# Kernel optimization log

Measured on AMD Instinct MI355X. Metric: run time of the kernel, lower is better.

Reference implementation:

```python
import jax, jax.numpy as jnp
import numpy as np

B, C, OC, H, W = 2, 64, 128, 96, 96
HD, DI, N, R, K = C // 2, C, 16, 2, 4  # VSSBlock: hidden=C/2, d_inner=2*hidden=C, d_state, dt_rank, 4 scan dirs
EPS = 1e-5


def _conv(x, w, b, pad, groups=1):
    y = jax.lax.conv_general_dilated(x, w, (1, 1), pad, feature_group_count=groups,
                                     dimension_numbers=('NCHW', 'OIHW', 'NCHW'))
    return y + b[None, :, None, None]


def _ln(x, w, b):
    m = x.mean(-1, keepdims=True)
    v = x.var(-1, keepdims=True)
    return (x - m) * jax.lax.rsqrt(v + EPS) * w + b


def _selective_scan(xs, dts, Bs, Cs, A, D):
    # xs, dts: (B,K,DI,L); Bs, Cs: (B,K,N,L); A: (K,DI,N); D: (K,DI)
    dts = jax.nn.softplus(dts)

    def step(h, inp):
        u_t, dt_t, B_t, C_t = inp
        dA = jnp.exp(dt_t[..., None] * A)                         # (B,K,DI,N)
        h = dA * h + (dt_t * u_t)[..., None] * B_t[:, :, None, :]
        return h, jnp.einsum('bkdn,bkn->bkd', h, C_t)

    seq = (jnp.moveaxis(xs, -1, 0), jnp.moveaxis(dts, -1, 0),
           jnp.moveaxis(Bs, -1, 0), jnp.moveaxis(Cs, -1, 0))
    h0 = jnp.zeros(xs.shape[:3] + (A.shape[-1],), xs.dtype)
    _, ys = jax.lax.scan(step, h0, seq)
    return jnp.moveaxis(ys, 0, -1) + D[None, :, :, None] * xs


def _vss_block(x, ln_w, ln_b, in_w, conv_w, conv_b, xproj_w, dtproj_w, dtproj_b,
               A_logs, Ds, on_w, on_b, out_w):
    # x: (B,H,W,HD); VMamba SS2D with 4-direction cross-scan + residual
    b, hh, ww, _ = x.shape
    L = hh * ww
    h = _ln(x, ln_w, ln_b)
    xz = h @ in_w                                   # (B,H,W,2*DI)
    xp, z = jnp.split(xz, 2, axis=-1)
    xc = jnp.transpose(xp, (0, 3, 1, 2))            # (B,DI,H,W)
    xc = jax.nn.silu(_conv(xc, conv_w, conv_b, ((1, 1), (1, 1)), groups=DI))
    x_flat = xc.reshape(b, DI, L)
    x_wh = jnp.transpose(xc, (0, 1, 3, 2)).reshape(b, DI, L)
    x2 = jnp.stack([x_flat, x_wh], axis=1)
    xs = jnp.concatenate([x2, jnp.flip(x2, -1)], axis=1)      # (B,4,DI,L)
    x_dbl = jnp.einsum('bkdl,kcd->bkcl', xs, xproj_w)
    dts, Bs, Cs = jnp.split(x_dbl, [R, R + N], axis=2)
    dts = jnp.einsum('bkrl,kdr->bkdl', dts, dtproj_w) + dtproj_b[None, :, :, None]
    A = -jnp.exp(A_logs)
    ys = _selective_scan(xs, dts, Bs, Cs, A, Ds)              # (B,4,DI,L)
    inv = jnp.flip(ys[:, 2:4], -1)
    unwh = lambda t: jnp.transpose(t.reshape(b, DI, ww, hh), (0, 1, 3, 2)).reshape(b, DI, L)
    y = ys[:, 0] + inv[:, 0] + unwh(ys[:, 1]) + unwh(inv[:, 1])
    y = jnp.transpose(y.reshape(b, DI, hh, ww), (0, 2, 3, 1))
    y = _ln(y, on_w, on_b) * jax.nn.silu(z)
    return x + y @ out_w


def _forward(x, ms_dw33_w, ms_dw33_b, ms_in_w, ms_in_b, ms_scale,
             vss_ln_w, vss_ln_b, vss_in_w, vss_conv_w, vss_conv_b, vss_xproj_w,
             vss_dtproj_w, vss_dtproj_b, vss_A_logs, vss_Ds, vss_on_w, vss_on_b, vss_out_w,
             ma_conv_w, ma_conv_b, adw_h_w, adw_h_b, adw_w_w, adw_w_b,
             pw_w, pw_b, bn_w, bn_b, bn_mean, bn_var):
    vss = (vss_ln_w, vss_ln_b, vss_in_w, vss_conv_w, vss_conv_b, vss_xproj_w,
           vss_dtproj_w, vss_dtproj_b, vss_A_logs, vss_Ds, vss_on_w, vss_on_b, vss_out_w)
    # --- MambaSplit (shared VSSBlock applied to both channel halves) ---
    xd = _conv(x, ms_dw33_w, ms_dw33_b, ((1, 1), (1, 1)), groups=C)
    x1, x2 = jnp.split(xd, 2, axis=1)

    def branch(xp):
        y = _vss_block(jnp.transpose(xp, (0, 2, 3, 1)), *vss)
        return ms_scale * xp + jnp.transpose(y, (0, 3, 1, 2))

    xm = jnp.concatenate([branch(x1), branch(x2)], axis=1)
    m = xm.mean((2, 3), keepdims=True)
    v = xm.var((2, 3), keepdims=True)
    xm = (xm - m) * jax.lax.rsqrt(v + EPS) * ms_in_w[None, :, None, None] + ms_in_b[None, :, None, None]
    xm = jax.nn.leaky_relu(xm, 0.01)
    # --- MaxAvg (global avg+max pool -> 3x3 conv on 1x1 map -> sigmoid gate) ---
    pooled = jnp.concatenate([x.mean((2, 3), keepdims=True), x.max((2, 3), keepdims=True)], axis=1)
    gate = jax.nn.sigmoid(_conv(pooled, ma_conv_w, ma_conv_b, ((1, 1), (1, 1))))
    xs_ = xm + gate * x
    # --- AxialDW ---
    xs_ = xs_ + _conv(xs_, adw_h_w, adw_h_b, ((1, 1), (0, 0)), groups=C) \
              + _conv(xs_, adw_w_w, adw_w_b, ((0, 0), (1, 1)), groups=C)
    # --- BN (eval) + ReLU, 1x1 conv, 2x2 maxpool ---
    skip = jax.nn.relu((xs_ - bn_mean[None, :, None, None]) * jax.lax.rsqrt(bn_var[None, :, None, None] + EPS)
                       * bn_w[None, :, None, None] + bn_b[None, :, None, None])
    out = _conv(skip, pw_w, pw_b, ((0, 0), (0, 0)))
    down = jax.lax.reduce_window(out, -jnp.inf, jax.lax.max, (1, 1, 2, 2), (1, 1, 2, 2), 'VALID')
    return down, skip


def setup_inputs() -> dict:
    key = jax.random.key(0)
    ks = jax.random.split(key, 16)
    r = lambda i, shape, s=0.02: jax.random.normal(ks[i], shape, jnp.float32) * s
    return {
        'x': jax.random.normal(ks[0], (B, C, H, W), jnp.float32),
        'ms_dw33_w': r(1, (C, 1, 3, 3), 0.1), 'ms_dw33_b': jnp.zeros(C),
        'ms_in_w': jnp.ones(C), 'ms_in_b': jnp.zeros(C),
        'ms_scale': jnp.ones((1,)),
        'vss_ln_w': jnp.ones(HD), 'vss_ln_b': jnp.zeros(HD),
        'vss_in_w': r(2, (HD, 2 * DI)),
        'vss_conv_w': r(3, (DI, 1, 3, 3), 0.1), 'vss_conv_b': jnp.zeros(DI),
        'vss_xproj_w': r(4, (K, R + 2 * N, DI)),
        'vss_dtproj_w': r(5, (K, DI, R), 0.1), 'vss_dtproj_b': r(6, (K, DI), 0.1),
        'vss_A_logs': jnp.tile(jnp.log(jnp.arange(1, N + 1, dtype=jnp.float32)), (K, DI, 1)),
        'vss_Ds': jnp.ones((K, DI)),
        'vss_on_w': jnp.ones(DI), 'vss_on_b': jnp.zeros(DI),
        'vss_out_w': r(7, (DI, HD)),
        'ma_conv_w': r(8, (C, 2 * C, 3, 3), 0.05), 'ma_conv_b': jnp.zeros(C),
        'adw_h_w': r(9, (C, 1, 3, 1), 0.1), 'adw_h_b': jnp.zeros(C),
        'adw_w_w': r(10, (C, 1, 1, 3), 0.1), 'adw_w_b': jnp.zeros(C),
        'pw_w': r(11, (OC, C, 1, 1)), 'pw_b': jnp.zeros(OC),
        'bn_w': jnp.ones(C), 'bn_b': jnp.zeros(C),
        'bn_mean': jnp.zeros(C), 'bn_var': jnp.ones(C),
    }


def reference(x, ms_dw33_w, ms_dw33_b, ms_in_w, ms_in_b, ms_scale,
              vss_ln_w, vss_ln_b, vss_in_w, vss_conv_w, vss_conv_b, vss_xproj_w,
              vss_dtproj_w, vss_dtproj_b, vss_A_logs, vss_Ds, vss_on_w, vss_on_b, vss_out_w,
              ma_conv_w, ma_conv_b, adw_h_w, adw_h_b, adw_w_w, adw_w_b,
              pw_w, pw_b, bn_w, bn_b, bn_mean, bn_var):
    return _forward(x, ms_dw33_w, ms_dw33_b, ms_in_w, ms_in_b, ms_scale,
                    vss_ln_w, vss_ln_b, vss_in_w, vss_conv_w, vss_conv_b, vss_xproj_w,
                    vss_dtproj_w, vss_dtproj_b, vss_A_logs, vss_Ds, vss_on_w, vss_on_b, vss_out_w,
                    ma_conv_w, ma_conv_b, adw_h_w, adw_h_b, adw_w_w, adw_w_b,
                    pw_w, pw_b, bn_w, bn_b, bn_mean, bn_var)
```

## Files before the change

kernel.cpp:

```cpp
#include <hip/hip_runtime.h>
#include <hip/hip_bf16.h>

typedef __hip_bfloat16 bf16;
#define DEV __device__ __forceinline__

constexpr int B_ = 2, C_ = 64, H_ = 96, W_ = 96, L_ = 9216;
constexpr int HD_ = 32, DI_ = 64, N_ = 16, K_ = 4, BB_ = 4;
constexpr int OC_ = 128;
constexpr int CH_ = 384, CL_ = 24;
constexpr int XST = 36;
constexpr float EPSF = 1e-5f;
constexpr int DOWN_SZ = B_ * OC_ * 48 * 48;

typedef __attribute__((ext_vector_type(8))) short short8;
typedef __attribute__((ext_vector_type(4))) float f32x4;

DEV float softplusf(float x) { return x > 15.f ? x : __logf(1.f + __expf(x)); }
DEV float b2f(bf16 v) { return __bfloat162float(v); }

__constant__ float kLogN[16] = {
  0.0f, 0.69314718f, 1.09861229f, 1.38629436f, 1.60943791f, 1.79175947f,
  1.94591015f, 2.07944154f, 2.19722458f, 2.30258509f, 2.39789527f,
  2.48490665f, 2.56494936f, 2.63905733f, 2.70805020f, 2.77258872f};

DEV void chunk_addr(int k, int chunk, int& idx0, int& stride) {
  int r4 = chunk & 3, q = chunk >> 2;
  if (k == 0)      { idx0 = chunk * CL_;                        stride = 1;   }
  else if (k == 1) { idx0 = (24 * r4) * 96 + q;                 stride = 96;  }
  else if (k == 2) { idx0 = L_ - 1 - chunk * CL_;               stride = -1;  }
  else             { idx0 = (95 - 24 * r4) * 96 + (95 - q);     stride = -96; }
}

DEV void pow_tree(float e1, float* ep) {
  float e2 = e1 * e1, e4 = e2 * e2, e8 = e4 * e4;
  float e3 = e2 * e1, e5 = e4 * e1, e6 = e4 * e2, e7 = e4 * e3;
  ep[0] = e1;  ep[1] = e2;  ep[2] = e3;  ep[3] = e4;
  ep[4] = e5;  ep[5] = e6;  ep[6] = e7;  ep[7] = e8;
  ep[8] = e8 * e1;  ep[9] = e8 * e2;  ep[10] = e8 * e3;  ep[11] = e8 * e4;
  ep[12] = e8 * e5; ep[13] = e8 * e6; ep[14] = e8 * e7;  ep[15] = e8 * e8;
}

DEV void ld_b(const float* __restrict__ xdb, const bf16* __restrict__ xcb, int d, int idx,
              float& t0, float& t1, float& u, float* Bv) {
  int uidx = __builtin_amdgcn_readfirstlane(idx);
  const float* p = xdb + (size_t)uidx * XST;
  t0 = p[0]; t1 = p[1];
  u = b2f(xcb[(size_t)idx * DI_ + d]);
  *(float4*)&Bv[0]  = *(const float4*)(p + 4);
  *(float4*)&Bv[4]  = *(const float4*)(p + 8);
  *(float4*)&Bv[8]  = *(const float4*)(p + 12);
  *(float4*)&Bv[12] = *(const float4*)(p + 16);
}
DEV void ld_bc(const float* __restrict__ xdb, const bf16* __restrict__ xcb, int d, int idx,
               float& t0, float& t1, float& u, float* Bv, float* Cv) {
  int uidx = __builtin_amdgcn_readfirstlane(idx);
  const float* p = xdb + (size_t)uidx * XST;
  t0 = p[0]; t1 = p[1];
  u = b2f(xcb[(size_t)idx * DI_ + d]);
  *(float4*)&Bv[0]  = *(const float4*)(p + 4);
  *(float4*)&Bv[4]  = *(const float4*)(p + 8);
  *(float4*)&Bv[8]  = *(const float4*)(p + 12);
  *(float4*)&Bv[12] = *(const float4*)(p + 16);
  *(float4*)&Cv[0]  = *(const float4*)(p + 20);
  *(float4*)&Cv[4]  = *(const float4*)(p + 24);
  *(float4*)&Cv[8]  = *(const float4*)(p + 28);
  *(float4*)&Cv[12] = *(const float4*)(p + 32);
}

DEV void step1(float t0, float t1, float u, const float* Bv,
               float w0, float w1, float bia, float A1, float& S, float* h) {
  float dt = softplusf(fmaf(t0, w0, fmaf(t1, w1, bia)));
  S += dt;
  float du = dt * u;
  float ep[16];
  pow_tree(__expf(dt * A1), ep);
#pragma unroll
  for (int n = 0; n < N_; n++) h[n] = fmaf(ep[n], h[n], du * Bv[n]);
}

DEV float step3(float t0, float t1, float u, const float* Bv, const float* Cv,
                float w0, float w1, float bia, float A1, float Dk, float* h) {
  float dt = softplusf(fmaf(t0, w0, fmaf(t1, w1, bia)));
  float du = dt * u;
  float ep[16];
  pow_tree(__expf(dt * A1), ep);
  float m[16];
#pragma unroll
  for (int n = 0; n < N_; n++) {
    h[n] = fmaf(ep[n], h[n], du * Bv[n]);
    m[n] = h[n] * Cv[n];
  }
  float a0 = m[0] + m[1], a1 = m[2] + m[3], a2 = m[4] + m[5], a3 = m[6] + m[7];
  float a4 = m[8] + m[9], a5 = m[10] + m[11], a6 = m[12] + m[13], a7 = m[14] + m[15];
  float b0 = a0 + a1, b1 = a2 + a3, b2 = a4 + a5, b3 = a6 + a7;
  return fmaf(Dk, u, (b0 + b1) + (b2 + b3));
}

__global__ void k_dw33(const float* __restrict__ x, const float* __restrict__ w,
                       const float* __restrict__ bias, float* __restrict__ out) {
  int t = blockIdx.x * 256 + threadIdx.x;
  if (t >= B_ * C_ * L_) return;
  int wi = t % W_, hi = (t / W_) % H_, c = (t / L_) % C_;
  float acc = bias[c];
#pragma unroll
  for (int dy = -1; dy <= 1; dy++) {
    int hh = hi + dy; if (hh < 0 || hh >= H_) continue;
#pragma unroll
    for (int dx = -1; dx <= 1; dx++) {
      int ww = wi + dx; if (ww < 0 || ww >= W_) continue;
      acc = fmaf(x[t + dy * W_ + dx], w[c * 9 + (dy + 1) * 3 + (dx + 1)], acc);
    }
  }
  out[t] = acc;
}

__global__ __launch_bounds__(256, 4) void k_ln_inproj(
    const float* __restrict__ xd, const float* __restrict__ lnw,
    const float* __restrict__ lnb, const float* __restrict__ inw,
    float* __restrict__ xzA, float* __restrict__ xzB) {
  int bb = blockIdx.y, t = threadIdx.x;
  int b = bb & 1, co = (bb >> 1) * HD_;
  int idx0 = blockIdx.x * 64;
  __shared__ float xds[32 * 68];
  __shared__ float meanA[64], rstdA[64];
  int lane = t & 63;
  for (int r = 0; r < 8; r++) {
    int c = r * 4 + (t >> 6);
    xds[c * 68 + lane] = xd[(size_t)(b * C_ + co + c) * L_ + idx0 + lane];
  }
  __syncthreads();
  if (t < 64) {
    float s = 0.f, sq = 0.f;
#pragma unroll
    for (int c = 0; c < 32; c++) { float v = xds[c * 68 + t]; s += v; sq = fmaf(v, v, sq); }
    float mean = s * (1.f / HD_);
    float var = sq * (1.f / HD_) - mean * mean;
    meanA[t] = mean; rstdA[t] = rsqrtf(var + EPSF);
  }
  __syncthreads();
  for (int i = t; i < 2048; i += 256) {
    int c = i >> 6, idx = i & 63;
    float v = xds[c * 68 + idx];
    xds[c * 68 + idx] = (v - meanA[idx]) * rstdA[idx] * lnw[c] + lnb[c];
  }
  __syncthreads();
  int oc = t & 127, g = t >> 7;
  float acc[32];
#pragma unroll
  for (int j = 0; j < 32; j++) acc[j] = 0.f;
  for (int c = 0; c < 32; c++) {
    float wv = inw[c * 128 + oc];
    const float4* row = reinterpret_cast<const float4*>(&xds[c * 68 + g * 32]);
#pragma unroll
    for (int j4 = 0; j4 < 8; j4++) {
      float4 xv = row[j4];
      acc[j4 * 4 + 0] = fmaf(xv.x, wv, acc[j4 * 4 + 0]);
      acc[j4 * 4 + 1] = fmaf(xv.y, wv, acc[j4 * 4 + 1]);
      acc[j4 * 4 + 2] = fmaf(xv.z, wv, acc[j4 * 4 + 2]);
      acc[j4 * 4 + 3] = fmaf(xv.w, wv, acc[j4 * 4 + 3]);
    }
  }
  float* dst = (oc < 64) ? xzA : xzB;
  int occ = oc & 63;
#pragma unroll
  for (int j = 0; j < 32; j++) {
    int idx = g * 32 + j;
    dst[(size_t)(bb * L_ + idx0 + idx) * 64 + occ] = acc[j];
  }
}

__global__ void k_dwsilu(const float* __restrict__ xzA, const float* __restrict__ cw,
                         const float* __restrict__ cb, bf16* __restrict__ xch) {
  int t = blockIdx.x * 256 + threadIdx.x;
  int d = t & 63, idx = (t >> 6) % L_, bb = t / (L_ * DI_);
  int wi = idx % W_, hi = idx / W_;
  float acc = cb[d];
#pragma unroll
  for (int dy = -1; dy <= 1; dy++) {
    int hh = hi + dy; if (hh < 0 || hh >= H_) continue;
#pragma unroll
    for (int dx = -1; dx <= 1; dx++) {
      int ww = wi + dx; if (ww < 0 || ww >= W_) continue;
      acc = fmaf(xzA[(size_t)(bb * L_ + hh * W_ + ww) * 64 + d],
                 cw[d * 9 + (dy + 1) * 3 + (dx + 1)], acc);
    }
  }
  acc = acc / (1.f + __expf(-acc));
  xch[t] = __float2bfloat16(acc);
}

__global__ void k_wprep(const float* __restrict__ xpw, bf16* __restrict__ wh) {
  int i = blockIdx.x * 256 + threadIdx.x;
  if (i >= 144 * 64) return;
  int n = i >> 6;
  wh[i] = __float2bfloat16(n < 136 ? xpw[i] : 0.f);
}

__global__ __launch_bounds__(256, 4) void k_xdbl_mfma(
    const bf16* __restrict__ xch, const bf16* __restrict__ wh,
    float* __restrict__ xdbl) {
  int w = threadIdx.x >> 6, lane = threadIdx.x & 63;
  int bb = blockIdx.y;
  int mtile = blockIdx.x * 4 + w;
  int idx0 = mtile * 16;
  int m = lane & 15, quad = lane >> 4;
  const bf16* arow = xch + ((size_t)bb * L_ + idx0 + m) * 64 + quad * 8;
  short8 a0 = *reinterpret_cast<const short8*>(arow);
  short8 a1 = *reinterpret_cast<const short8*>(arow + 32);
#pragma unroll
  for (int nt = 0; nt < 9; nt++) {
    int n = nt * 16 + m;
    const bf16* brow = wh + n * 64 + quad * 8;
    short8 b0 = *reinterpret_cast<const short8*>(brow);
    short8 b1 = *reinterpret_cast<const short8*>(brow + 32);
    f32x4 acc = {0.f, 0.f, 0.f, 0.f};
    acc = __builtin_amdgcn_mfma_f32_16x16x32_bf16(a0, b0, acc, 0, 0, 0);
    acc = __builtin_amdgcn_mfma_f32_16x16x32_bf16(a1, b1, acc, 0, 0, 0);
    if (n < 136) {
      int k4 = (n >= 102) ? 3 : (n >= 68) ? 2 : (n >= 34) ? 1 : 0;
      int c = n - k4 * 34;
      int col = (c < 2) ? c : c + 2;
      float* dst = xdbl + ((size_t)(bb * K_ + k4) * L_ + idx0 + quad * 4) * XST + col;
      dst[0] = acc[0]; dst[XST] = acc[1]; dst[2 * XST] = acc[2]; dst[3 * XST] = acc[3];
    }
  }
}

__global__ __launch_bounds__(256, 4) void k_scan1(
    const float* __restrict__ xdbl, const bf16* __restrict__ xch,
    const float* __restrict__ dtw, const float* __restrict__ dtb,
    const float* __restrict__ alog, bf16* __restrict__ hbuf,
    float* __restrict__ ssum) {
  int w = threadIdx.x >> 6, d = threadIdx.x & 63;
  int chunk = blockIdx.x * 4 + w, k = blockIdx.y, bb = blockIdx.z;
  float w0 = dtw[(k * DI_ + d) * 2 + 0], w1 = dtw[(k * DI_ + d) * 2 + 1];
  float bia = dtb[k * DI_ + d];
  const float* al = alog + (k * DI_ + d) * N_;
  float a0 = al[0];
  bool lin = true;
#pragma unroll
  for (int n = 1; n < N_; n++) lin = lin && (fabsf(al[n] - a0 - kLogN[n]) < 3e-5f);
  bool chain = (__ballot(lin) == ~0ull);
  float A1 = -__expf(a0);
  float h[N_];
#pragma unroll
  for (int n = 0; n < N_; n++) h[n] = 0.f;
  int idx0, stride;
  chunk_addr(k, chunk, idx0, stride);
  const float* xdb = xdbl + (size_t)(bb * K_ + k) * L_ * XST;
  const bf16* xcb = xch + (size_t)bb * L_ * DI_;
  float S = 0.f;
  if (chain) {
    float t0a, t1a, ua, Ba[16];
    float t0b, t1b, ub, Bb[16];
    int ia = idx0;
    ld_b(xdb, xcb, d, ia, t0a, t1a, ua, Ba);
    for (int s = 0; s < CL_; s += 2) {
      int ib = ia + stride;
      ld_b(xdb, xcb, d, ib, t0b, t1b, ub, Bb);
      step1(t0a, t1a, ua, Ba, w0, w1, bia, A1, S, h);
      int in2 = (s + 2 < CL_) ? ib + stride : idx0;
      ld_b(xdb, xcb, d, in2, t0a, t1a, ua, Ba);
      step1(t0b, t1b, ub, Bb, w0, w1, bia, A1, S, h);
      ia = in2;
    }
  } else {
    float A[N_];
#pragma unroll
    for (int n = 0; n < N_; n++) A[n] = -__expf(al[n]);
    int idx = idx0;
    for (int s = 0; s < CL_; s++) {
      float t0, t1, u, Bv[16];
      ld_b(xdb, xcb, d, idx, t0, t1, u, Bv);
      float dt = softplusf(fmaf(t0, w0, fmaf(t1, w1, bia)));
      S += dt;
      float du = dt * u;
#pragma unroll
      for (int n = 0; n < N_; n++) h[n] = fmaf(__expf(dt * A[n]), h[n], du * Bv[n]);
      idx += stride;
    }
  }
  size_t base = (size_t)((bb * K_ + k) * CH_ + chunk) * DI_ + d;
  ssum[base] = S;
#pragma unroll
  for (int n = 0; n < N_; n++) hbuf[base * N_ + n] = __float2bfloat16(h[n]);
}

__global__ void k_scan2(const float* __restrict__ alog, const float* __restrict__ ssum,
                        bf16* __restrict__ hbuf) {
  int t = blockIdx.x * 256 + threadIdx.x;
  int n = t & 15, d = (t >> 4) & 63, kk = (t >> 10) & 3, bb = t >> 12;
  float A = -__expf(alog[(kk * DI_ + d) * N_ + n]);
  size_t row = (size_t)(bb * K_ + kk) * CH_ * DI_ + d;
  constexpr int U = 16;
  float Sb[U], hb[U];
#pragma unroll
  for (int j = 0; j < U; j++) {
    size_t sb = row + (size_t)j * DI_;
    Sb[j] = ssum[sb]; hb[j] = b2f(hbuf[sb * N_ + n]);
  }
  float hp = 0.f;
  for (int c = 0; c < CH_; c += U) {
    float S2[U], h2[U];
    if (c + U < CH_) {
#pragma unroll
      for (int j = 0; j < U; j++) {
        size_t sb = row + (size_t)(c + U + j) * DI_;
        S2[j] = ssum[sb]; h2[j] = b2f(hbuf[sb * N_ + n]);
      }
    } else {
#pragma unroll
      for (int j = 0; j < U; j++) { S2[j] = 0.f; h2[j] = 0.f; }
    }
#pragma unroll
    for (int j = 0; j < U; j++) {
      size_t sb = row + (size_t)(c + j) * DI_;
      float e = __expf(A * Sb[j]);
      hbuf[sb * N_ + n] = __float2bfloat16(hp);
      hp = fmaf(e, hp, hb[j]);
    }
#pragma unroll
    for (int j = 0; j < U; j++) { Sb[j] = S2[j]; hb[j] = h2[j]; }
  }
}

__global__ __launch_bounds__(256, 4) void k_scan3(
    const float* __restrict__ xdbl, const bf16* __restrict__ xch,
    const float* __restrict__ dtw, const float* __restrict__ dtb,
    const float* __restrict__ alog, const float* __restrict__ Dsw,
    const bf16* __restrict__ hbuf, bf16* __restrict__ ydir) {
  int w = threadIdx.x >> 6, d = threadIdx.x & 63;
  int chunk = blockIdx.x * 4 + w, k = blockIdx.y, bb = blockIdx.z;
  float w0 = dtw[(k * DI_ + d) * 2 + 0], w1 = dtw[(k * DI_ + d) * 2 + 1];
  float bia = dtb[k * DI_ + d];
  float Dk = Dsw[k * DI_ + d];
  const float* al = alog + (k * DI_ + d) * N_;
  float a0 = al[0];
  bool lin = true;
#pragma unroll
  for (int n = 1; n < N_; n++) lin = lin && (fabsf(al[n] - a0 - kLogN[n]) < 3e-5f);
  bool chain = (__ballot(lin) == ~0ull);
  float A1 = -__expf(a0);
  float h[N_];
  size_t base = (size_t)((bb * K_ + k) * CH_ + chunk) * DI_ + d;
#pragma unroll
  for (int n = 0; n < N_; n++) h[n] = b2f(hbuf[base * N_ + n]);
  int idx0, stride;
  chunk_addr(k, chunk, idx0, stride);
  const float* xdb = xdbl + (size_t)(bb * K_ + k) * L_ * XST;
  const bf16* xcb = xch + (size_t)bb * L_ * DI_;
  bf16* yb = ydir + (size_t)(bb * K_ + k) * L_ * DI_;
  if (chain) {
    float t0a, t1a, ua, Ba[16], Ca[16];
    float t0b, t1b, ub, Bb[16], Cb[16];
    int ia = idx0;
    ld_bc(xdb, xcb, d, ia, t0a, t1a, ua, Ba, Ca);
    for (int s = 0; s < CL_; s += 2) {
      int ib = ia + stride;
      ld_bc(xdb, xcb, d, ib, t0b, t1b, ub, Bb, Cb);
      float y = step3(t0a, t1a, ua, Ba, Ca, w0, w1, bia, A1, Dk, h);
      yb[(size_t)ia * DI_ + d] = __float2bfloat16(y);
      int in2 = (s + 2 < CL_) ? ib + stride : idx0;
      ld_bc(xdb, xcb, d, in2, t0a, t1a, ua, Ba, Ca);
      y = step3(t0b, t1b, ub, Bb, Cb, w0, w1, bia, A1, Dk, h);
      yb[(size_t)ib * DI_ + d] = __float2bfloat16(y);
      ia = in2;
    }
  } else {
    float A[N_];
#pragma unroll
    for (int n = 0; n < N_; n++) A[n] = -__expf(al[n]);
    int idx = idx0;
    for (int s = 0; s < CL_; s++) {
      float t0, t1, u, Bv[16], Cv[16];
      ld_bc(xdb, xcb, d, idx, t0, t1, u, Bv, Cv);
      float dt = softplusf(fmaf(t0, w0, fmaf(t1, w1, bia)));
      float du = dt * u;
      float y = 0.f;
#pragma unroll
      for (int n = 0; n < N_; n++) {
        h[n] = fmaf(__expf(dt * A[n]), h[n], du * Bv[n]);
        y = fmaf(h[n], Cv[n], y);
      }
      y = fmaf(Dk, u, y);
      yb[(size_t)idx * DI_ + d] = __float2bfloat16(y);
      idx += stride;
    }
  }
}

__global__ void k_combine(const bf16* __restrict__ ydir, const float* __restrict__ xzB,
                          const float* __restrict__ xd, const float* __restrict__ onw,
                          const float* __restrict__ onb, const float* __restrict__ outw,
                          const float* __restrict__ mssc, float* __restrict__ xm) {
  int w = threadIdx.x >> 6, d = threadIdx.x & 63;
  int idx = blockIdx.x * 4 + w, bb = blockIdx.y;
  int b = bb & 1, co = (bb >> 1) * HD_;
  const bf16* yd = ydir + (size_t)bb * K_ * L_ * DI_;
  size_t off = (size_t)idx * DI_ + d;
  float y = b2f(yd[off]) + b2f(yd[(size_t)L_ * DI_ + off])
          + b2f(yd[(size_t)2 * L_ * DI_ + off]) + b2f(yd[(size_t)3 * L_ * DI_ + off]);
  float s = y, sq = y * y;
#pragma unroll
  for (int m = 1; m < 64; m <<= 1) { s += __shfl_xor(s, m, 64); sq += __shfl_xor(sq, m, 64); }
  float mean = s * (1.f / DI_);
  float var = sq * (1.f / DI_) - mean * mean;
  float rstd = rsqrtf(var + EPSF);
  float yn = (y - mean) * rstd * onw[d] + onb[d];
  float z = xzB[(size_t)(bb * L_ + idx) * 64 + d];
  float g = yn * (z / (1.f + __expf(-z)));
  __shared__ float gs[4][DI_];
  gs[w][d] = g;
  __syncthreads();
  if (d < HD_) {
    float acc = 0.f;
#pragma unroll
    for (int dd = 0; dd < DI_; dd++) acc = fmaf(gs[w][dd], outw[dd * HD_ + d], acc);
    size_t xi = (size_t)(b * C_ + co + d) * L_ + idx;
    float xp = xd[xi];
    xm[xi] = mssc[0] * xp + xp + acc;
  }
}

__global__ __launch_bounds__(1024) void k_stats(
    const float* __restrict__ xm, const float* __restrict__ x,
    float* __restrict__ inm, float* __restrict__ inr,
    float* __restrict__ xmean, float* __restrict__ xmax) {
  int bc = blockIdx.x, t = threadIdx.x;
  const float* pm = xm + (size_t)bc * L_;
  const float* px = x + (size_t)bc * L_;
  float s = 0.f, sq = 0.f, xs = 0.f, mx = -1e30f;
  for (int i = t; i < L_; i += 1024) {
    float v = pm[i]; s += v; sq = fmaf(v, v, sq);
    float xv = px[i]; xs += xv; mx = fmaxf(mx, xv);
  }
  __shared__ float red[64];
#pragma unroll
  for (int m = 1; m < 64; m <<= 1) {
    s += __shfl_xor(s, m, 64); sq += __shfl_xor(sq, m, 64);
    xs += __shfl_xor(xs, m, 64); mx = fmaxf(mx, __shfl_xor(mx, m, 64));
  }
  int wid = t >> 6;
  if ((t & 63) == 0) { red[wid] = s; red[16 + wid] = sq; red[32 + wid] = xs; red[48 + wid] = mx; }
  __syncthreads();
  if (t == 0) {
    s = 0.f; sq = 0.f; xs = 0.f; mx = -1e30f;
#pragma unroll
    for (int i = 0; i < 16; i++) {
      s += red[i]; sq += red[16 + i]; xs += red[32 + i]; mx = fmaxf(mx, red[48 + i]);
    }
    float mean = s * (1.f / L_);
    float var = sq * (1.f / L_) - mean * mean;
    inm[bc] = mean;
    inr[bc] = rsqrtf(var + EPSF);
    xmean[bc] = xs * (1.f / L_);
    xmax[bc] = mx;
  }
}

__global__ void k_xs(const float* __restrict__ xm, const float* __restrict__ inm,
                     const float* __restrict__ inr, const float* __restrict__ msw,
                     const float* __restrict__ msb, const float* __restrict__ xmean,
                     const float* __restrict__ xmax, const float* __restrict__ maw,
                     const float* __restrict__ mab, const float* __restrict__ x,
                     float* __restrict__ xs2) {
  int t = blockIdx.x * 256 + threadIdx.x;
  int bc = t / L_, c = bc & 63, b = bc >> 6;
  __shared__ float gsh;
  if (threadIdx.x < 64) {
    int ic = threadIdx.x;
    float p = xmean[b * 64 + ic] * maw[(c * 128 + ic) * 9 + 4]
            + xmax[b * 64 + ic] * maw[(c * 128 + 64 + ic) * 9 + 4];
#pragma unroll
    for (int m = 1; m < 64; m <<= 1) p += __shfl_xor(p, m, 64);
    if (ic == 0) gsh = 1.f / (1.f + __expf(-(p + mab[c])));
  }
  __syncthreads();
  float gate = gsh;
  float v = xm[t];
  v = (v - inm[bc]) * inr[bc] * msw[c] + msb[c];
  v = v > 0.f ? v : 0.01f * v;
  xs2[t] = v + gate * x[t];
}

__global__ void k_axbn(const float* __restrict__ xs2, const float* __restrict__ hw,
                       const float* __restrict__ hb, const float* __restrict__ wwt,
                       const float* __restrict__ wb, const float* __restrict__ bnw,
                       const float* __restrict__ bnb, const float* __restrict__ bnm,
                       const float* __restrict__ bnv, float* __restrict__ skipo) {
  int t = blockIdx.x * 256 + threadIdx.x;
  if (t >= B_ * C_ * L_) return;
  int wi = t % W_, hi = (t / W_) % H_, c = (t / L_) % C_;
  float a = xs2[t];
  float hacc = hb[c];
#pragma unroll
  for (int dy = -1; dy <= 1; dy++) {
    int hh = hi + dy; if (hh < 0 || hh >= H_) continue;
    hacc = fmaf(xs2[t + dy * W_], hw[c * 3 + dy + 1], hacc);
  }
  float wacc = wb[c];
#pragma unroll
  for (int dx = -1; dx <= 1; dx++) {
    int ww = wi + dx; if (ww < 0 || ww >= W_) continue;
    wacc = fmaf(xs2[t + dx], wwt[c * 3 + dx + 1], wacc);
  }
  float v = a + hacc + wacc;
  float sv = (v - bnm[c]) * rsqrtf(bnv[c] + EPSF) * bnw[c] + bnb[c];
  skipo[t] = fmaxf(sv, 0.f);
}

__global__ void k_pwpool(const float* __restrict__ skipo, const float* __restrict__ pww,
                         const float* __restrict__ pwb, float* __restrict__ down) {
  int h2 = blockIdx.x, b = blockIdx.y, t = threadIdx.x;
  int oc0 = blockIdx.z * 32;
  __shared__ float sk[64 * 192];
  for (int i = t; i < 64 * 192; i += 256) {
    int c = i / 192, rw = i % 192, r = rw / 96, wcol = rw % 96;
    sk[i] = skipo[((size_t)(b * C_ + c) * H_ + (2 * h2 + r)) * W_ + wcol];
  }
  __syncthreads();
  for (int o = t; o < 32 * 48; o += 256) {
    int oc = oc0 + o / 48, w2 = o % 48;
    float s0 = 0.f, s1 = 0.f, s2 = 0.f, s3 = 0.f;
#pragma unroll 8
    for (int c = 0; c < 64; c++) {
      float wv = pww[oc * 64 + c];
      const float* sp = &sk[c * 192 + 2 * w2];
      s0 = fmaf(sp[0], wv, s0);
      s1 = fmaf(sp[1], wv, s1);
      s2 = fmaf(sp[96], wv, s2);
      s3 = fmaf(sp[97], wv, s3);
    }
    float v = fmaxf(fmaxf(s0, s1), fmaxf(s2, s3)) + pwb[oc];
    down[((size_t)(b * OC_ + oc) * 48 + h2) * 48 + w2] = v;
  }
}

extern "C" void kernel_launch(void* const* d_in, const int* in_sizes, int n_in,
                              void* d_out, int out_size, void* d_ws, size_t ws_size,
                              hipStream_t stream) {
  const float* x     = (const float*)d_in[0];
  const float* dw33w = (const float*)d_in[1];
  const float* dw33b = (const float*)d_in[2];
  const float* msw   = (const float*)d_in[3];
  const float* msb   = (const float*)d_in[4];
  const float* mssc  = (const float*)d_in[5];
  const float* lnw   = (const float*)d_in[6];
  const float* lnb   = (const float*)d_in[7];
  const float* inw   = (const float*)d_in[8];
  const float* cw    = (const float*)d_in[9];
  const float* cb    = (const float*)d_in[10];
  const float* xpw   = (const float*)d_in[11];
  const float* dtw   = (const float*)d_in[12];
  const float* dtb   = (const float*)d_in[13];
  const float* alog  = (const float*)d_in[14];
  const float* Dsw   = (const float*)d_in[15];
  const float* onw   = (const float*)d_in[16];
  const float* onb   = (const float*)d_in[17];
  const float* outw  = (const float*)d_in[18];
  const float* maw   = (const float*)d_in[19];
  const float* mab   = (const float*)d_in[20];
  const float* ahw   = (const float*)d_in[21];
  const float* ahb   = (const float*)d_in[22];
  const float* aww   = (const float*)d_in[23];
  const float* awb   = (const float*)d_in[24];
  const float* pww   = (const float*)d_in[25];
  const float* pwb   = (const float*)d_in[26];
  const float* bnw   = (const float*)d_in[27];
  const float* bnb   = (const float*)d_in[28];
  const float* bnm   = (const float*)d_in[29];
  const float* bnv   = (const float*)d_in[30];

  float* ws = (float*)d_ws;
  float* xd   = ws;
  float* xzA  = xd + 1179648;
  bf16*  hbuf = (bf16*)xzA;
  float* xzB  = xzA + 3145728;
  float* xdbl = xzB + 2359296;
  float* ssum = xdbl + 5308416;
  bf16*  ydir = (bf16*)(ssum + 393216);
  float* xm   = ssum + 393216 + 4718592;
  float* xs2  = xm + 1179648;
  bf16*  xch  = (bf16*)xs2;
  float* st   = xs2 + 1179648;
  float* inm = st, *inr = st + 128, *xmean = st + 256, *xmaxv = st + 384;
  bf16*  wh   = (bf16*)(st + 512);

  float* outp = (float*)d_out;
  float* down = outp;
  float* skipo = outp + DOWN_SZ;

  dim3 b256(256);
  int nEl = B_ * C_ * L_;

  k_wprep<<<dim3(36), b256, 0, stream>>>(xpw, wh);
  k_dw33<<<dim3((nEl + 255) / 256), b256, 0, stream>>>(x, dw33w, dw33b, xd);
  k_ln_inproj<<<dim3(L_ / 64, BB_), b256, 0, stream>>>(xd, lnw, lnb, inw, xzA, xzB);
  k_dwsilu<<<dim3(BB_ * L_ * DI_ / 256), b256, 0, stream>>>(xzA, cw, cb, xch);
  k_xdbl_mfma<<<dim3(L_ / 64, BB_), b256, 0, stream>>>(xch, wh, xdbl);
  k_scan1<<<dim3(CH_ / 4, K_, BB_), b256, 0, stream>>>(xdbl, xch, dtw, dtb, alog, hbuf, ssum);
  k_scan2<<<dim3(BB_ * K_ * DI_ * N_ / 256), b256, 0, stream>>>(alog, ssum, hbuf);
  k_scan3<<<dim3(CH_ / 4, K_, BB_), b256, 0, stream>>>(xdbl, xch, dtw, dtb, alog, Dsw, hbuf, ydir);
  k_combine<<<dim3(L_ / 4, BB_), b256, 0, stream>>>(ydir, xzB, xd, onw, onb, outw, mssc, xm);
  k_stats<<<dim3(B_ * C_), dim3(1024), 0, stream>>>(xm, x, inm, inr, xmean, xmaxv);
  k_xs<<<dim3((nEl + 255) / 256), b256, 0, stream>>>(xm, inm, inr, msw, msb, xmean, xmaxv, maw, mab, x, xs2);
  k_axbn<<<dim3((nEl + 255) / 256), b256, 0, stream>>>(xs2, ahw, ahb, aww, awb, bnw, bnb, bnm, bnv, skipo);
  k_pwpool<<<dim3(48, B_, 4), b256, 0, stream>>>(skipo, pww, pwb, down);
}
```

Before: 344.0 us.

## Fold scan pass 3 into combine via carry-in correction with bf16 B/C

Restructures the chunked selective scan from three passes to two. The first pass now also emits local outputs and cumulative dt, and the combine kernel adds the carry-in contribution C·exp(A·S)·h_prev per direction. This removes a full second sweep over the sequence. It also packs B and C projections and the z gate as bf16 and precomputes A/linearity flags once in the weight-prep kernel. This reduces memory traffic and redundant exp work, at the cost of extra bf16 rounding in B, C and the cumulative-dt term, and more gather work in combine.

```diff
diff --git a/kernel.cpp b/kernel.cpp
--- a/kernel.cpp
+++ b/kernel.cpp
@@ -8,7 +8,6 @@
 constexpr int HD_ = 32, DI_ = 64, N_ = 16, K_ = 4, BB_ = 4;
 constexpr int OC_ = 128;
 constexpr int CH_ = 384, CL_ = 24;
-constexpr int XST = 36;
 constexpr float EPSF = 1e-5f;
 constexpr int DOWN_SZ = B_ * OC_ * 48 * 48;
 
@@ -17,6 +16,14 @@
 
 DEV float softplusf(float x) { return x > 15.f ? x : __logf(1.f + __expf(x)); }
 DEV float b2f(bf16 v) { return __bfloat162float(v); }
+DEV float lo16f(unsigned v) { return __uint_as_float(v << 16); }
+DEV float hi16f(unsigned v) { return __uint_as_float(v & 0xffff0000u); }
+DEV void unpk(uint4 a, uint4 b, float* v) {
+  v[0] = lo16f(a.x); v[1] = hi16f(a.x); v[2] = lo16f(a.y); v[3] = hi16f(a.y);
+  v[4] = lo16f(a.z); v[5] = hi16f(a.z); v[6] = lo16f(a.w); v[7] = hi16f(a.w);
+  v[8] = lo16f(b.x); v[9] = hi16f(b.x); v[10] = lo16f(b.y); v[11] = hi16f(b.y);
+  v[12] = lo16f(b.z); v[13] = hi16f(b.z); v[14] = lo16f(b.w); v[15] = hi16f(b.w);
+}
 
 __constant__ float kLogN[16] = {
   0.0f, 0.69314718f, 1.09861229f, 1.38629436f, 1.60943791f, 1.79175947f,
@@ -40,50 +47,29 @@
   ep[12] = e8 * e5; ep[13] = e8 * e6; ep[14] = e8 * e7;  ep[15] = e8 * e8;
 }
 
-DEV void ld_b(const float* __restrict__ xdb, const bf16* __restrict__ xcb, int d, int idx,
-              float& t0, float& t1, float& u, float* Bv) {
-  int uidx = __builtin_amdgcn_readfirstlane(idx);
-  const float* p = xdb + (size_t)uidx * XST;
-  t0 = p[0]; t1 = p[1];
+DEV void ldrow(const float* __restrict__ bB, const bf16* __restrict__ bC,
+               const bf16* __restrict__ xcb, int d, int idx,
+               uint4& qb0, uint4& qb1, uint4& qc0, uint4& qc1,
+               float& t0, float& t1, float& u) {
+  int uix = __builtin_amdgcn_readfirstlane(idx);
+  const float* p = bB + (size_t)uix * 12;
+  qb0 = *(const uint4*)p; qb1 = *(const uint4*)(p + 4);
+  t0 = p[8]; t1 = p[9];
+  const uint4* cq = (const uint4*)(bC + (size_t)uix * 16);
+  qc0 = cq[0]; qc1 = cq[1];
   u = b2f(xcb[(size_t)idx * DI_ + d]);
-  *(float4*)&Bv[0]  = *(const float4*)(p + 4);
-  *(float4*)&Bv[4]  = *(const float4*)(p + 8);
-  *(float4*)&Bv[8]  = *(const float4*)(p + 12);
-  *(float4*)&Bv[12] = *(const float4*)(p + 16);
-}
-DEV void ld_bc(const float* __restrict__ xdb, const bf16* __restrict__ xcb, int d, int idx,
-               float& t0, float& t1, float& u, float* Bv, float* Cv) {
-  int uidx = __builtin_amdgcn_readfirstlane(idx);
-  const float* p = xdb + (size_t)uidx * XST;
-  t0 = p[0]; t1 = p[1];
-  u = b2f(xcb[(size_t)idx * DI_ + d]);
-  *(float4*)&Bv[0]  = *(const float4*)(p + 4);
-  *(float4*)&Bv[4]  = *(const float4*)(p + 8);
-  *(float4*)&Bv[8]  = *(const float4*)(p + 12);
-  *(float4*)&Bv[12] = *(const float4*)(p + 16);
-  *(float4*)&Cv[0]  = *(const float4*)(p + 20);
-  *(float4*)&Cv[4]  = *(const float4*)(p + 24);
-  *(float4*)&Cv[8]  = *(const float4*)(p + 28);
-  *(float4*)&Cv[12] = *(const float4*)(p + 32);
-}
-
-DEV void step1(float t0, float t1, float u, const float* Bv,
-               float w0, float w1, float bia, float A1, float& S, float* h) {
+}
+
+DEV void pstep(uint4 qb0, uint4 qb1, uint4 qc0, uint4 qc1, float t0, float t1, float u,
+               float w0, float w1, float bia, float A1, float Dk,
+               float* h, float& S, float& yout) {
+  float Bv[16], Cv[16];
+  unpk(qb0, qb1, Bv); unpk(qc0, qc1, Cv);
   float dt = softplusf(fmaf(t0, w0, fmaf(t1, w1, bia)));
   S += dt;
   float du = dt * u;
   float ep[16];
   pow_tree(__expf(dt * A1), ep);
-#pragma unroll
-  for (int n = 0; n < N_; n++) h[n] = fmaf(ep[n], h[n], du * Bv[n]);
-}
-
-DEV float step3(float t0, float t1, float u, const float* Bv, const float* Cv,
-                float w0, float w1, float bia, float A1, float Dk, float* h) {
-  float dt = softplusf(fmaf(t0, w0, fmaf(t1, w1, bia)));
-  float du = dt * u;
-  float ep[16];
-  pow_tree(__expf(dt * A1), ep);
   float m[16];
 #pragma unroll
   for (int n = 0; n < N_; n++) {
@@ -93,7 +79,7 @@
   float a0 = m[0] + m[1], a1 = m[2] + m[3], a2 = m[4] + m[5], a3 = m[6] + m[7];
   float a4 = m[8] + m[9], a5 = m[10] + m[11], a6 = m[12] + m[13], a7 = m[14] + m[15];
   float b0 = a0 + a1, b1 = a2 + a3, b2 = a4 + a5, b3 = a6 + a7;
-  return fmaf(Dk, u, (b0 + b1) + (b2 + b3));
+  yout = fmaf(Dk, u, (b0 + b1) + (b2 + b3));
 }
 
 __global__ void k_dw33(const float* __restrict__ x, const float* __restrict__ w,
@@ -117,7 +103,7 @@
 __global__ __launch_bounds__(256, 4) void k_ln_inproj(
     const float* __restrict__ xd, const float* __restrict__ lnw,
     const float* __restrict__ lnb, const float* __restrict__ inw,
-    float* __restrict__ xzA, float* __restrict__ xzB) {
+    float* __restrict__ xzA, bf16* __restrict__ xzBh) {
   int bb = blockIdx.y, t = threadIdx.x;
   int b = bb & 1, co = (bb >> 1) * HD_;
   int idx0 = blockIdx.x * 64;
@@ -160,12 +146,15 @@
       acc[j4 * 4 + 3] = fmaf(xv.w, wv, acc[j4 * 4 + 3]);
     }
   }
-  float* dst = (oc < 64) ? xzA : xzB;
   int occ = oc & 63;
-#pragma unroll
-  for (int j = 0; j < 32; j++) {
-    int idx = g * 32 + j;
-    dst[(size_t)(bb * L_ + idx0 + idx) * 64 + occ] = acc[j];
+  if (oc < 64) {
+#pragma unroll
+    for (int j = 0; j < 32; j++)
+      xzA[(size_t)(bb * L_ + idx0 + g * 32 + j) * 64 + occ] = acc[j];
+  } else {
+#pragma unroll
+    for (int j = 0; j < 32; j++)
+      xzBh[(size_t)(bb * L_ + idx0 + g * 32 + j) * 64 + occ] = __float2bfloat16(acc[j]);
   }
 }
 
@@ -189,16 +178,30 @@
   xch[t] = __float2bfloat16(acc);
 }
 
-__global__ void k_wprep(const float* __restrict__ xpw, bf16* __restrict__ wh) {
+__global__ void k_wprep(const float* __restrict__ xpw, const float* __restrict__ alog,
+                        bf16* __restrict__ wh, float* __restrict__ aux) {
   int i = blockIdx.x * 256 + threadIdx.x;
-  if (i >= 144 * 64) return;
-  int n = i >> 6;
-  wh[i] = __float2bfloat16(n < 136 ? xpw[i] : 0.f);
+  if (i < 144 * 64) {
+    int n = i >> 6;
+    wh[i] = __float2bfloat16(n < 136 ? xpw[i] : 0.f);
+  }
+  if (blockIdx.x == 0 && threadIdx.x < 256) {
+    int kd = threadIdx.x;
+    const float* al = alog + kd * N_;
+    float a0 = al[0];
+    bool lin = true;
+#pragma unroll
+    for (int n = 1; n < N_; n++) lin = lin && (fabsf(al[n] - a0 - kLogN[n]) < 3e-5f);
+    aux[kd] = -__expf(a0);
+    aux[256 + kd] = lin ? 1.f : 0.f;
+#pragma unroll
+    for (int n = 0; n < N_; n++) aux[512 + kd * N_ + n] = -__expf(al[n]);
+  }
 }
 
 __global__ __launch_bounds__(256, 4) void k_xdbl_mfma(
     const bf16* __restrict__ xch, const bf16* __restrict__ wh,
-    float* __restrict__ xdbl) {
+    float* __restrict__ xdblB, bf16* __restrict__ xdblC) {
   int w = threadIdx.x >> 6, lane = threadIdx.x & 63;
   int bb = blockIdx.y;
   int mtile = blockIdx.x * 4 + w;
@@ -219,162 +222,78 @@
     if (n < 136) {
       int k4 = (n >= 102) ? 3 : (n >= 68) ? 2 : (n >= 34) ? 1 : 0;
       int c = n - k4 * 34;
-      int col = (c < 2) ? c : c + 2;
-      float* dst = xdbl + ((size_t)(bb * K_ + k4) * L_ + idx0 + quad * 4) * XST + col;
-      dst[0] = acc[0]; dst[XST] = acc[1]; dst[2 * XST] = acc[2]; dst[3 * XST] = acc[3];
+      size_t row = (size_t)(bb * K_ + k4) * L_ + idx0 + quad * 4;
+      if (c < 2) {
+        float* db = xdblB + row * 12 + 8 + c;
+        db[0] = acc[0]; db[12] = acc[1]; db[24] = acc[2]; db[36] = acc[3];
+      } else if (c < 18) {
+        bf16* bp = (bf16*)(xdblB + row * 12) + (c - 2);
+        bp[0] = __float2bfloat16(acc[0]);  bp[24] = __float2bfloat16(acc[1]);
+        bp[48] = __float2bfloat16(acc[2]); bp[72] = __float2bfloat16(acc[3]);
+      } else {
+        bf16* cp = xdblC + row * 16 + (c - 18);
+        cp[0] = __float2bfloat16(acc[0]);  cp[16] = __float2bfloat16(acc[1]);
+        cp[32] = __float2bfloat16(acc[2]); cp[48] = __float2bfloat16(acc[3]);
+      }
     }
   }
 }
 
 __global__ __launch_bounds__(256, 4) void k_scan1(
-    const float* __restrict__ xdbl, const bf16* __restrict__ xch,
-    const float* __restrict__ dtw, const float* __restrict__ dtb,
-    const float* __restrict__ alog, bf16* __restrict__ hbuf,
-    float* __restrict__ ssum) {
-  int w = threadIdx.x >> 6, d = threadIdx.x & 63;
-  int chunk = blockIdx.x * 4 + w, k = blockIdx.y, bb = blockIdx.z;
-  float w0 = dtw[(k * DI_ + d) * 2 + 0], w1 = dtw[(k * DI_ + d) * 2 + 1];
-  float bia = dtb[k * DI_ + d];
-  const float* al = alog + (k * DI_ + d) * N_;
-  float a0 = al[0];
-  bool lin = true;
-#pragma unroll
-  for (int n = 1; n < N_; n++) lin = lin && (fabsf(al[n] - a0 - kLogN[n]) < 3e-5f);
-  bool chain = (__ballot(lin) == ~0ull);
-  float A1 = -__expf(a0);
-  float h[N_];
-#pragma unroll
-  for (int n = 0; n < N_; n++) h[n] = 0.f;
-  int idx0, stride;
-  chunk_addr(k, chunk, idx0, stride);
-  const float* xdb = xdbl + (size_t)(bb * K_ + k) * L_ * XST;
-  const bf16* xcb = xch + (size_t)bb * L_ * DI_;
-  float S = 0.f;
-  if (chain) {
-    float t0a, t1a, ua, Ba[16];
-    float t0b, t1b, ub, Bb[16];
-    int ia = idx0;
-    ld_b(xdb, xcb, d, ia, t0a, t1a, ua, Ba);
-    for (int s = 0; s < CL_; s += 2) {
-      int ib = ia + stride;
-      ld_b(xdb, xcb, d, ib, t0b, t1b, ub, Bb);
-      step1(t0a, t1a, ua, Ba, w0, w1, bia, A1, S, h);
-      int in2 = (s + 2 < CL_) ? ib + stride : idx0;
-      ld_b(xdb, xcb, d, in2, t0a, t1a, ua, Ba);
-      step1(t0b, t1b, ub, Bb, w0, w1, bia, A1, S, h);
-      ia = in2;
-    }
-  } else {
-    float A[N_];
-#pragma unroll
-    for (int n = 0; n < N_; n++) A[n] = -__expf(al[n]);
-    int idx = idx0;
-    for (int s = 0; s < CL_; s++) {
-      float t0, t1, u, Bv[16];
-      ld_b(xdb, xcb, d, idx, t0, t1, u, Bv);
-      float dt = softplusf(fmaf(t0, w0, fmaf(t1, w1, bia)));
-      S += dt;
-      float du = dt * u;
-#pragma unroll
-      for (int n = 0; n < N_; n++) h[n] = fmaf(__expf(dt * A[n]), h[n], du * Bv[n]);
-      idx += stride;
-    }
-  }
-  size_t base = (size_t)((bb * K_ + k) * CH_ + chunk) * DI_ + d;
-  ssum[base] = S;
-#pragma unroll
-  for (int n = 0; n < N_; n++) hbuf[base * N_ + n] = __float2bfloat16(h[n]);
-}
-
-__global__ void k_scan2(const float* __restrict__ alog, const float* __restrict__ ssum,
-                        bf16* __restrict__ hbuf) {
-  int t = blockIdx.x * 256 + threadIdx.x;
-  int n = t & 15, d = (t >> 4) & 63, kk = (t >> 10) & 3, bb = t >> 12;
-  float A = -__expf(alog[(kk * DI_ + d) * N_ + n]);
-  size_t row = (size_t)(bb * K_ + kk) * CH_ * DI_ + d;
-  constexpr int U = 16;
-  float Sb[U], hb[U];
-#pragma unroll
-  for (int j = 0; j < U; j++) {
-    size_t sb = row + (size_t)j * DI_;
-    Sb[j] = ssum[sb]; hb[j] = b2f(hbuf[sb * N_ + n]);
-  }
-  float hp = 0.f;
-  for (int c = 0; c < CH_; c += U) {
-    float S2[U], h2[U];
-    if (c + U < CH_) {
-#pragma unroll
-      for (int j = 0; j < U; j++) {
-        size_t sb = row + (size_t)(c + U + j) * DI_;
-        S2[j] = ssum[sb]; h2[j] = b2f(hbuf[sb * N_ + n]);
-      }
-    } else {
-#pragma unroll
-      for (int j = 0; j < U; j++) { S2[j] = 0.f; h2[j] = 0.f; }
-    }
-#pragma unroll
-    for (int j = 0; j < U; j++) {
-      size_t sb = row + (size_t)(c + j) * DI_;
-      float e = __expf(A * Sb[j]);
-      hbuf[sb * N_ + n] = __float2bfloat16(hp);
-      hp = fmaf(e, hp, hb[j]);
-    }
-#pragma unroll
-    for (int j = 0; j < U; j++) { Sb[j] = S2[j]; hb[j] = h2[j]; }
-  }
-}
-
-__global__ __launch_bounds__(256, 4) void k_scan3(
-    const float* __restrict__ xdbl, const bf16* __restrict__ xch,
-    const float* __restrict__ dtw, const float* __restrict__ dtb,
-    const float* __restrict__ alog, const float* __restrict__ Dsw,
-    const bf16* __restrict__ hbuf, bf16* __restrict__ ydir) {
+    const float* __restrict__ xdblB, const bf16* __restrict__ xdblC,
+    const bf16* __restrict__ xch, const float* __restrict__ dtw,
+    const float* __restrict__ dtb, const float* __restrict__ Dsw,
+    const float* __restrict__ aux, bf16* __restrict__ hbuf,
+    float* __restrict__ ssum, bf16* __restrict__ ylocal, bf16* __restrict__ cdt) {
   int w = threadIdx.x >> 6, d = threadIdx.x & 63;
   int chunk = blockIdx.x * 4 + w, k = blockIdx.y, bb = blockIdx.z;
   float w0 = dtw[(k * DI_ + d) * 2 + 0], w1 = dtw[(k * DI_ + d) * 2 + 1];
   float bia = dtb[k * DI_ + d];
   float Dk = Dsw[k * DI_ + d];
-  const float* al = alog + (k * DI_ + d) * N_;
-  float a0 = al[0];
-  bool lin = true;
-#pragma unroll
-  for (int n = 1; n < N_; n++) lin = lin && (fabsf(al[n] - a0 - kLogN[n]) < 3e-5f);
-  bool chain = (__ballot(lin) == ~0ull);
-  float A1 = -__expf(a0);
+  float A1 = aux[k * 64 + d];
+  bool chain = (__ballot(aux[256 + k * 64 + d] > 0.5f) == ~0ull);
   float h[N_];
-  size_t base = (size_t)((bb * K_ + k) * CH_ + chunk) * DI_ + d;
-#pragma unroll
-  for (int n = 0; n < N_; n++) h[n] = b2f(hbuf[base * N_ + n]);
+#pragma unroll
+  for (int n = 0; n < N_; n++) h[n] = 0.f;
   int idx0, stride;
   chunk_addr(k, chunk, idx0, stride);
-  const float* xdb = xdbl + (size_t)(bb * K_ + k) * L_ * XST;
+  const float* bB = xdblB + (size_t)(bb * K_ + k) * L_ * 12;
+  const bf16* bC = xdblC + (size_t)(bb * K_ + k) * L_ * 16;
   const bf16* xcb = xch + (size_t)bb * L_ * DI_;
-  bf16* yb = ydir + (size_t)(bb * K_ + k) * L_ * DI_;
+  bf16* yb = ylocal + (size_t)(bb * K_ + k) * L_ * DI_;
+  bf16* cb2 = cdt + (size_t)(bb * K_ + k) * L_ * DI_;
+  float S = 0.f;
   if (chain) {
-    float t0a, t1a, ua, Ba[16], Ca[16];
-    float t0b, t1b, ub, Bb[16], Cb[16];
+    uint4 qb0a, qb1a, qc0a, qc1a; float t0a, t1a, ua;
+    uint4 qb0b, qb1b, qc0b, qc1b; float t0b, t1b, ub;
     int ia = idx0;
-    ld_bc(xdb, xcb, d, ia, t0a, t1a, ua, Ba, Ca);
+    ldrow(bB, bC, xcb, d, ia, qb0a, qb1a, qc0a, qc1a, t0a, t1a, ua);
     for (int s = 0; s < CL_; s += 2) {
       int ib = ia + stride;
-      ld_bc(xdb, xcb, d, ib, t0b, t1b, ub, Bb, Cb);
-      float y = step3(t0a, t1a, ua, Ba, Ca, w0, w1, bia, A1, Dk, h);
+      ldrow(bB, bC, xcb, d, ib, qb0b, qb1b, qc0b, qc1b, t0b, t1b, ub);
+      float y;
+      pstep(qb0a, qb1a, qc0a, qc1a, t0a, t1a, ua, w0, w1, bia, A1, Dk, h, S, y);
       yb[(size_t)ia * DI_ + d] = __float2bfloat16(y);
+      cb2[(size_t)ia * DI_ + d] = __float2bfloat16(S);
       int in2 = (s + 2 < CL_) ? ib + stride : idx0;
-      ld_bc(xdb, xcb, d, in2, t0a, t1a, ua, Ba, Ca);
-      y = step3(t0b, t1b, ub, Bb, Cb, w0, w1, bia, A1, Dk, h);
+      ldrow(bB, bC, xcb, d, in2, qb0a, qb1a, qc0a, qc1a, t0a, t1a, ua);
+      pstep(qb0b, qb1b, qc0b, qc1b, t0b, t1b, ub, w0, w1, bia, A1, Dk, h, S, y);
       yb[(size_t)ib * DI_ + d] = __float2bfloat16(y);
+      cb2[(size_t)ib * DI_ + d] = __float2bfloat16(S);
       ia = in2;
     }
   } else {
     float A[N_];
 #pragma unroll
-    for (int n = 0; n < N_; n++) A[n] = -__expf(al[n]);
+    for (int n = 0; n < N_; n++) A[n] = aux[512 + (k * 64 + d) * N_ + n];
     int idx = idx0;
     for (int s = 0; s < CL_; s++) {
-      float t0, t1, u, Bv[16], Cv[16];
-      ld_bc(xdb, xcb, d, idx, t0, t1, u, Bv, Cv);
+      uint4 qb0, qb1, qc0, qc1; float t0, t1, u;
+      ldrow(bB, bC, xcb, d, idx, qb0, qb1, qc0, qc1, t0, t1, u);
+      float Bv[16], Cv[16];
+      unpk(qb0, qb1, Bv); unpk(qc0, qc1, Cv);
       float dt = softplusf(fmaf(t0, w0, fmaf(t1, w1, bia)));
+      S += dt;
       float du = dt * u;
       float y = 0.f;
 #pragma unroll
@@ -384,22 +303,103 @@
       }
       y = fmaf(Dk, u, y);
       yb[(size_t)idx * DI_ + d] = __float2bfloat16(y);
+      cb2[(size_t)idx * DI_ + d] = __float2bfloat16(S);
       idx += stride;
     }
   }
-}
-
-__global__ void k_combine(const bf16* __restrict__ ydir, const float* __restrict__ xzB,
-                          const float* __restrict__ xd, const float* __restrict__ onw,
-                          const float* __restrict__ onb, const float* __restrict__ outw,
-                          const float* __restrict__ mssc, float* __restrict__ xm) {
+  size_t base = (size_t)((bb * K_ + k) * CH_ + chunk) * DI_ + d;
+  ssum[base] = S;
+#pragma unroll
+  for (int n = 0; n < N_; n++) hbuf[base * N_ + n] = __float2bfloat16(h[n]);
+}
+
+__global__ void k_scan2(const float* __restrict__ aux, const float* __restrict__ ssum,
+                        bf16* __restrict__ hbuf) {
+  int t = blockIdx.x * 256 + threadIdx.x;
+  int n = t & 15, d = (t >> 4) & 63, kk = (t >> 10) & 3, bb = t >> 12;
+  float A = aux[512 + (kk * 64 + d) * N_ + n];
+  size_t row = (size_t)(bb * K_ + kk) * CH_ * DI_ + d;
+  constexpr int U = 16;
+  float Sb[U], hb[U];
+#pragma unroll
+  for (int j = 0; j < U; j++) {
+    size_t sb = row + (size_t)j * DI_;
+    Sb[j] = ssum[sb]; hb[j] = b2f(hbuf[sb * N_ + n]);
+  }
+  float hp = 0.f;
+  for (int c = 0; c < CH_; c += U) {
+    float S2[U], h2[U];
+    if (c + U < CH_) {
+#pragma unroll
+      for (int j = 0; j < U; j++) {
+        size_t sb = row + (size_t)(c + U + j) * DI_;
+        S2[j] = ssum[sb]; h2[j] = b2f(hbuf[sb * N_ + n]);
+      }
+    } else {
+#pragma unroll
+      for (int j = 0; j < U; j++) { S2[j] = 0.f; h2[j] = 0.f; }
+    }
+#pragma unroll
+    for (int j = 0; j < U; j++) {
+      size_t sb = row + (size_t)(c + j) * DI_;
+      float e = __expf(A * Sb[j]);
+      hbuf[sb * N_ + n] = __float2bfloat16(hp);
+      hp = fmaf(e, hp, hb[j]);
+    }
+#pragma unroll
+    for (int j = 0; j < U; j++) { Sb[j] = S2[j]; hb[j] = h2[j]; }
+  }
+}
+
+__global__ __launch_bounds__(256, 4) void k_combine(
+    const bf16* __restrict__ ylocal, const bf16* __restrict__ cdt,
+    const bf16* __restrict__ hbuf, const bf16* __restrict__ xdblC,
+    const float* __restrict__ aux, const bf16* __restrict__ xzBh,
+    const float* __restrict__ xd, const float* __restrict__ onw,
+    const float* __restrict__ onb, const float* __restrict__ outw,
+    const float* __restrict__ mssc, float* __restrict__ xm) {
   int w = threadIdx.x >> 6, d = threadIdx.x & 63;
   int idx = blockIdx.x * 4 + w, bb = blockIdx.y;
   int b = bb & 1, co = (bb >> 1) * HD_;
-  const bf16* yd = ydir + (size_t)bb * K_ * L_ * DI_;
-  size_t off = (size_t)idx * DI_ + d;
-  float y = b2f(yd[off]) + b2f(yd[(size_t)L_ * DI_ + off])
-          + b2f(yd[(size_t)2 * L_ * DI_ + off]) + b2f(yd[(size_t)3 * L_ * DI_ + off]);
+  int hii = idx / 96, wii = idx - hii * 96;
+  int lt = wii * 96 + hii;
+  int lk[4] = { idx, lt, L_ - 1 - idx, L_ - 1 - lt };
+  float y = 0.f;
+#pragma unroll
+  for (int k = 0; k < K_; k++) {
+    int chunk = lk[k] / CL_;
+    size_t row = (size_t)(bb * K_ + k) * L_ + idx;
+    float yk = b2f(ylocal[row * DI_ + d]);
+    float S = b2f(cdt[row * DI_ + d]);
+    float A1 = aux[k * 64 + d];
+    bool chain = (__ballot(aux[256 + k * 64 + d] > 0.5f) == ~0ull);
+    const bf16* hb = hbuf + ((size_t)((bb * K_ + k) * CH_ + chunk) * DI_ + d) * N_;
+    uint4 qh0 = *(const uint4*)hb, qh1 = *(const uint4*)(hb + 8);
+    float hv[16];
+    unpk(qh0, qh1, hv);
+    const uint4* cq = (const uint4*)(xdblC + row * 16);
+    float Cv[16];
+    unpk(cq[0], cq[1], Cv);
+    float corr;
+    if (chain) {
+      float ep[16];
+      pow_tree(__expf(A1 * S), ep);
+      float m[16];
+#pragma unroll
+      for (int n = 0; n < N_; n++) m[n] = Cv[n] * (ep[n] * hv[n]);
+      float a0 = m[0] + m[1], a1 = m[2] + m[3], a2 = m[4] + m[5], a3 = m[6] + m[7];
+      float a4 = m[8] + m[9], a5 = m[10] + m[11], a6 = m[12] + m[13], a7 = m[14] + m[15];
+      corr = ((a0 + a1) + (a2 + a3)) + ((a4 + a5) + (a6 + a7));
+    } else {
+      corr = 0.f;
+#pragma unroll
+      for (int n = 0; n < N_; n++) {
+        float A = aux[512 + (k * 64 + d) * N_ + n];
+        corr = fmaf(Cv[n] * hv[n], __expf(A * S), corr);
+      }
+    }
+    y += yk + corr;
+  }
   float s = y, sq = y * y;
 #pragma unroll
   for (int m = 1; m < 64; m <<= 1) { s += __shfl_xor(s, m, 64); sq += __shfl_xor(sq, m, 64); }
@@ -407,7 +407,7 @@
   float var = sq * (1.f / DI_) - mean * mean;
   float rstd = rsqrtf(var + EPSF);
   float yn = (y - mean) * rstd * onw[d] + onb[d];
-  float z = xzB[(size_t)(bb * L_ + idx) * 64 + d];
+  float z = b2f(xzBh[(size_t)(bb * L_ + idx) * 64 + d]);
   float g = yn * (z / (1.f + __expf(-z)));
   __shared__ float gs[4][DI_];
   gs[w][d] = g;
@@ -572,19 +572,23 @@
   const float* bnv   = (const float*)d_in[30];
 
   float* ws = (float*)d_ws;
-  float* xd   = ws;
-  float* xzA  = xd + 1179648;
-  bf16*  hbuf = (bf16*)xzA;
-  float* xzB  = xzA + 3145728;
-  float* xdbl = xzB + 2359296;
-  float* ssum = xdbl + 5308416;
-  bf16*  ydir = (bf16*)(ssum + 393216);
-  float* xm   = ssum + 393216 + 4718592;
-  float* xs2  = xm + 1179648;
-  bf16*  xch  = (bf16*)xs2;
-  float* st   = xs2 + 1179648;
+  float* xd    = ws;
+  float* xzA   = xd + 1179648;
+  bf16*  hbuf  = (bf16*)xzA;
+  bf16*  xzBh  = (bf16*)(xzA + 3145728);
+  float* xdblB = xzA + 3145728 + 1179648;
+  bf16*  xdblC = (bf16*)(xdblB + 1769472);
+  float* ssum  = xdblB + 1769472 + 1179648;
+  bf16*  ylocal = (bf16*)(ssum + 393216);
+  bf16*  cdt   = (bf16*)(ssum + 393216 + 4718592);
+  float* xmR   = ssum + 393216 + 4718592 + 4718592;
+  bf16*  xch   = (bf16*)xmR;
+  float* xm    = xmR;
+  float* xs2   = (float*)ylocal;
+  float* st    = xmR + 1179648;
   float* inm = st, *inr = st + 128, *xmean = st + 256, *xmaxv = st + 384;
-  bf16*  wh   = (bf16*)(st + 512);
+  float* aux   = st + 512;
+  bf16*  wh    = (bf16*)(aux + 4608);
 
   float* outp = (float*)d_out;
   float* down = outp;
@@ -593,15 +597,16 @@
   dim3 b256(256);
   int nEl = B_ * C_ * L_;
 
-  k_wprep<<<dim3(36), b256, 0, stream>>>(xpw, wh);
+  k_wprep<<<dim3(36), b256, 0, stream>>>(xpw, alog, wh, aux);
   k_dw33<<<dim3((nEl + 255) / 256), b256, 0, stream>>>(x, dw33w, dw33b, xd);
-  k_ln_inproj<<<dim3(L_ / 64, BB_), b256, 0, stream>>>(xd, lnw, lnb, inw, xzA, xzB);
+  k_ln_inproj<<<dim3(L_ / 64, BB_), b256, 0, stream>>>(xd, lnw, lnb, inw, xzA, xzBh);
   k_dwsilu<<<dim3(BB_ * L_ * DI_ / 256), b256, 0, stream>>>(xzA, cw, cb, xch);
-  k_xdbl_mfma<<<dim3(L_ / 64, BB_), b256, 0, stream>>>(xch, wh, xdbl);
-  k_scan1<<<dim3(CH_ / 4, K_, BB_), b256, 0, stream>>>(xdbl, xch, dtw, dtb, alog, hbuf, ssum);
-  k_scan2<<<dim3(BB_ * K_ * DI_ * N_ / 256), b256, 0, stream>>>(alog, ssum, hbuf);
-  k_scan3<<<dim3(CH_ / 4, K_, BB_), b256, 0, stream>>>(xdbl, xch, dtw, dtb, alog, Dsw, hbuf, ydir);
-  k_combine<<<dim3(L_ / 4, BB_), b256, 0, stream>>>(ydir, xzB, xd, onw, onb, outw, mssc, xm);
+  k_xdbl_mfma<<<dim3(L_ / 64, BB_), b256, 0, stream>>>(xch, wh, xdblB, xdblC);
+  k_scan1<<<dim3(CH_ / 4, K_, BB_), b256, 0, stream>>>(xdblB, xdblC, xch, dtw, dtb, Dsw,
+                                                       aux, hbuf, ssum, ylocal, cdt);
+  k_scan2<<<dim3(BB_ * K_ * DI_ * N_ / 256), b256, 0, stream>>>(aux, ssum, hbuf);
+  k_combine<<<dim3(L_ / 4, BB_), b256, 0, stream>>>(ylocal, cdt, hbuf, xdblC, aux, xzBh,
+                                                    xd, onw, onb, outw, mssc, xm);
   k_stats<<<dim3(B_ * C_), dim3(1024), 0, stream>>>(xm, x, inm, inr, xmean, xmaxv);
   k_xs<<<dim3((nEl + 255) / 256), b256, 0, stream>>>(xm, inm, inr, msw, msb, xmean, xmaxv, maw, mab, x, xs2);
   k_axbn<<<dim3((nEl + 255) / 256), b256, 0, stream>>>(xs2, ahw, ahb, aww, awb, bnw, bnb, bnm, bnv, skipo);
```

Result: faster. 333.0 us (-3.2%).
